# Kernel tuning notes

Hardware: AMD Instinct MI355X
Metric: run time of the kernel (lower is better)

## Reference

```python
import jax, jax.numpy as jnp
import numpy as np


def setup_inputs() -> dict:
    key = jax.random.key(0)
    ks = jax.random.split(key, 6)
    B, L, D, E = 4, 2048, 1024, 4
    H = 4 * D
    x = jax.random.normal(ks[0], (B, L, D), dtype=jnp.float32)
    # router: Linear(D, 2D) -> GELU -> Linear(2D, E); kaiming-ish init
    rW1 = jax.random.normal(ks[1], (D, 2 * D), dtype=jnp.float32) * (2.0 / D) ** 0.5
    rb1 = jnp.zeros((2 * D,), dtype=jnp.float32)
    rW2 = jax.random.normal(ks[2], (2 * D, E), dtype=jnp.float32) * (2.0 / (2 * D)) ** 0.5
    rb2 = jnp.zeros((E,), dtype=jnp.float32)
    # experts: Linear(D, 4D) -> GELU -> Linear(4D, D), stacked over E
    We1 = jax.random.normal(ks[3], (E, D, H), dtype=jnp.float32) * (2.0 / D) ** 0.5
    be1 = jnp.zeros((E, H), dtype=jnp.float32)
    We2 = jax.random.normal(ks[4], (E, H, D), dtype=jnp.float32) * (2.0 / H) ** 0.5
    be2 = jnp.zeros((E, D), dtype=jnp.float32)
    return {"x": x, "rW1": rW1, "rb1": rb1, "rW2": rW2, "rb2": rb2,
            "We1": We1, "be1": be1, "We2": We2, "be2": be2}


def reference(x, rW1, rb1, rW2, rb2, We1, be1, We2, be2):
    E = We1.shape[0]
    top_k = min(2, E)
    # router (dropouts are identity in eval mode)
    rh = jax.nn.gelu(x @ rW1 + rb1, approximate=False)          # [B,L,2D]
    router_logits = rh @ rW2 + rb2                               # [B,L,E]
    router_probs = jax.nn.softmax(router_logits, axis=-1)
    expert_weights, expert_indices = jax.lax.top_k(router_probs, top_k)  # [B,L,k]
    one_hot = jax.nn.one_hot(expert_indices, E, dtype=x.dtype)   # [B,L,k,E]
    token_mask = one_hot.sum(axis=2)                             # [B,L,E] 1 if expert selected
    combine_w = (one_hot * expert_weights[..., None]).sum(axis=2)  # [B,L,E] gate weight per expert
    out = jnp.zeros_like(x)
    for e in range(E):  # fixed small expert count; dense per-expert MLP over all tokens (as original)
        xi = x * token_mask[..., e:e + 1]
        h = jax.nn.gelu(xi @ We1[e] + be1[e], approximate=False)  # [B,L,4D]
        yo = h @ We2[e] + be2[e]                                  # [B,L,D]
        out = out + yo * combine_w[..., e:e + 1]
    return out
```

## Files before the change

### kernel.cpp

```cpp
#include <hip/hip_runtime.h>
#include <math.h>


typedef short bf16x8 __attribute__((ext_vector_type(8)));
typedef float f32x4 __attribute__((ext_vector_type(4)));
typedef unsigned short u16;

__device__ __forceinline__ u16 f2bf(float f) {
  unsigned u = __float_as_uint(f);
  u += 0x7FFFu + ((u >> 16) & 1u);
  return (u16)(u >> 16);
}
__device__ __forceinline__ float bf2f(u16 s) {
  return __uint_as_float(((unsigned)s) << 16);
}
__device__ __forceinline__ float gelu_f(float x) {
  return 0.5f * x * (1.0f + erff(x * 0.70710678118654752f));
}
__device__ __forceinline__ float gelu_fast(float x) {
  float y = 1.5957691216057308f * (x + 0.044715f * x * x * x);
  float e = __expf(y);
  float t = 1.0f - 2.0f * __builtin_amdgcn_rcpf(e + 1.0f);
  return 0.5f * x * (1.0f + t);
}
__device__ __forceinline__ void gload_lds16(const void* g, void* l) {
  __builtin_amdgcn_global_load_lds(
      (const __attribute__((address_space(1))) void*)g,
      (__attribute__((address_space(3))) void*)l, 16, 0, 0);
}

__global__ __launch_bounds__(256) void convert_split_kernel(
    const float* __restrict__ in, u16* __restrict__ hi, u16* __restrict__ lo,
    int n4) {
  int i = blockIdx.x * blockDim.x + threadIdx.x;
  int stride = gridDim.x * blockDim.x;
  for (; i < n4; i += stride) {
    float4 v = ((const float4*)in)[i];
    float f[4] = {v.x, v.y, v.z, v.w};
    ushort4 h4, l4;
    u16* hp = (u16*)&h4;
    u16* lp = (u16*)&l4;
#pragma unroll
    for (int u = 0; u < 4; ++u) {
      u16 h = f2bf(f[u]);
      hp[u] = h;
      lp[u] = f2bf(f[u] - bf2f(h));
    }
    ((ushort4*)hi)[i] = h4;
    ((ushort4*)lo)[i] = l4;
  }
}

__global__ __launch_bounds__(256) void transpose_split_kernel(
    const float* __restrict__ in, u16* __restrict__ hi, u16* __restrict__ lo,
    int R, int C) {
  __shared__ float tile[32][33];
  const int c0 = blockIdx.x * 32, r0 = blockIdx.y * 32;
#pragma unroll
  for (int i = 0; i < 4; ++i) {
    int rr = threadIdx.y + i * 8;
    tile[rr][threadIdx.x] = in[(size_t)(r0 + rr) * C + c0 + threadIdx.x];
  }
  __syncthreads();
#pragma unroll
  for (int i = 0; i < 4; ++i) {
    int cc = threadIdx.y + i * 8;
    float v = tile[threadIdx.x][cc];
    u16 h = f2bf(v);
    size_t oidx = (size_t)(c0 + cc) * R + r0 + threadIdx.x;
    hi[oidx] = h;
    lo[oidx] = f2bf(v - bf2f(h));
  }
}

__global__ __launch_bounds__(256) void transpose_pair_kernel(
    const float* __restrict__ We1, const float* __restrict__ We2,
    u16* __restrict__ T1, u16* __restrict__ T2, size_t tstride, int e0) {
  __shared__ float tile[32][33];
  const int e = e0 + blockIdx.y;
  int b = blockIdx.x;
  const float* in;
  u16* out;
  int R, C, tx, ty;
  if (b < 4096) {
    in = We1 + (size_t)e * 1024 * 4096;
    out = T1 + (size_t)blockIdx.y * tstride;
    R = 1024; C = 4096; tx = b & 127; ty = b >> 7;
  } else {
    b -= 4096;
    in = We2 + (size_t)e * 1024 * 4096;
    out = T2 + (size_t)blockIdx.y * tstride;
    R = 4096; C = 1024; tx = b & 31; ty = b >> 5;
  }
  const int c0 = tx * 32, r0 = ty * 32;
#pragma unroll
  for (int i = 0; i < 4; ++i) {
    int rr = threadIdx.y + i * 8;
    tile[rr][threadIdx.x] = in[(size_t)(r0 + rr) * C + c0 + threadIdx.x];
  }
  __syncthreads();
#pragma unroll
  for (int i = 0; i < 4; ++i) {
    int cc = threadIdx.y + i * 8;
    out[(size_t)(c0 + cc) * R + r0 + threadIdx.x] = f2bf(tile[threadIdx.x][cc]);
  }
}

__global__ __launch_bounds__(256) void gemm3_router_kernel(
    const u16* __restrict__ Ahi, const u16* __restrict__ Alo,
    const u16* __restrict__ Bhi, const u16* __restrict__ Blo, int K,
    const float* __restrict__ bias, const float* __restrict__ rW2,
    float* __restrict__ parts) {
  __shared__ alignas(16) u16 Sm[4 * 128 * 32];
  __shared__ float pls[2][128][4];
  const int tid = threadIdx.x;
  const int lane = tid & 63;
  const int w = tid >> 6;
  const int wr = w >> 1, wc = w & 1;

  const int flat = blockIdx.x + blockIdx.y * 16;
  const int swz = (flat & 7) * 128 + (flat >> 3);
  const int bxs = swz & 15;
  const int bys = swz >> 4;
  const int brow = bys * 128;
  const int bcol = bxs * 128;

  f32x4 acc[4][4] = {};
  char* S = (char*)Sm;
  const u16* srcs[4] = {Ahi + (size_t)brow * K, Alo + (size_t)brow * K,
                        Bhi + (size_t)bcol * K, Blo + (size_t)bcol * K};
  const int rA = lane & 15;
  const int kg2 = (lane >> 4) * 16;

  const int nk = K >> 5;
  for (int kt = 0; kt < nk; ++kt) {
    const int k0 = kt << 5;
    __syncthreads();
#pragma unroll
    for (int i = 0; i < 8; ++i) {
      int c = tid + 256 * i;
      int tile = c >> 9;
      int cc = c & 511;
      int row = cc >> 2;
      int kp = (cc & 3) << 3;
      gload_lds16(srcs[tile] + (size_t)row * K + (k0 + kp), S + c * 16);
    }
    __syncthreads();

    bf16x8 ah[4], al[4], bh[4], bl[4];
#pragma unroll
    for (int m = 0; m < 4; ++m) {
      int ro = (wr * 64 + m * 16 + rA) * 64 + kg2;
      ah[m] = *(const bf16x8*)(S + ro);
      al[m] = *(const bf16x8*)(S + 8192 + ro);
    }
#pragma unroll
    for (int n = 0; n < 4; ++n) {
      int ro = (wc * 64 + n * 16 + rA) * 64 + kg2;
      bh[n] = *(const bf16x8*)(S + 16384 + ro);
      bl[n] = *(const bf16x8*)(S + 24576 + ro);
    }
#pragma unroll
    for (int m = 0; m < 4; ++m)
#pragma unroll
      for (int n = 0; n < 4; ++n) {
        acc[m][n] = __builtin_amdgcn_mfma_f32_16x16x32_bf16(ah[m], bh[n], acc[m][n], 0, 0, 0);
        acc[m][n] = __builtin_amdgcn_mfma_f32_16x16x32_bf16(al[m], bh[n], acc[m][n], 0, 0, 0);
        acc[m][n] = __builtin_amdgcn_mfma_f32_16x16x32_bf16(ah[m], bl[n], acc[m][n], 0, 0, 0);
      }
  }

  const int cr = (lane >> 4) * 4;
  const int ccx = lane & 15;
  float4 w2v[4];
  float bv[4];
#pragma unroll
  for (int n = 0; n < 4; ++n) {
    const int gc = bcol + wc * 64 + n * 16 + ccx;
    w2v[n] = ((const float4*)rW2)[gc];
    bv[n] = bias[gc];
  }
#pragma unroll
  for (int m = 0; m < 4; ++m) {
    float pl[4][4];
#pragma unroll
    for (int r = 0; r < 4; ++r)
#pragma unroll
      for (int e = 0; e < 4; ++e) pl[r][e] = 0.f;
#pragma unroll
    for (int n = 0; n < 4; ++n)
#pragma unroll
      for (int r = 0; r < 4; ++r) {
        const float v = gelu_f(acc[m][n][r] + bv[n]);
        pl[r][0] += v * w2v[n].x;
        pl[r][1] += v * w2v[n].y;
        pl[r][2] += v * w2v[n].z;
        pl[r][3] += v * w2v[n].w;
      }
#pragma unroll
    for (int off = 8; off; off >>= 1)
#pragma unroll
      for (int r = 0; r < 4; ++r)
#pragma unroll
        for (int e = 0; e < 4; ++e) pl[r][e] += __shfl_xor(pl[r][e], off);
    if ((lane & 15) == 0) {
      const int row = wr * 64 + m * 16 + cr;
#pragma unroll
      for (int r = 0; r < 4; ++r)
#pragma unroll
        for (int e = 0; e < 4; ++e) pls[wc][row + r][e] = pl[r][e];
    }
  }
  __syncthreads();
  for (int i = tid; i < 512; i += 256) {
    const int row = i >> 2, e = i & 3;
    parts[((size_t)bxs * 8192 + brow + row) * 4 + e] =
        pls[0][row][e] + pls[1][row][e];
  }
}

__global__ __launch_bounds__(256) void topk_kernel(
    const float* __restrict__ parts, const float* __restrict__ rb2,
    float* __restrict__ combine, int* __restrict__ cnt, int* __restrict__ list,
    int T) {
  const int t = blockIdx.x * 256 + threadIdx.x;
  const int w = threadIdx.x >> 6, lane = threadIdx.x & 63;
  __shared__ int wpre[4][4];
  __shared__ int gbase[4];

  float lg[4] = {rb2[0], rb2[1], rb2[2], rb2[3]};
#pragma unroll
  for (int s = 0; s < 16; ++s) {
    float4 pv = ((const float4*)parts)[(size_t)s * 8192 + t];
    lg[0] += pv.x;
    lg[1] += pv.y;
    lg[2] += pv.z;
    lg[3] += pv.w;
  }
  float mx = fmaxf(fmaxf(lg[0], lg[1]), fmaxf(lg[2], lg[3]));
  float p[4], sum = 0.f;
#pragma unroll
  for (int e = 0; e < 4; ++e) {
    p[e] = expf(lg[e] - mx);
    sum += p[e];
  }
  float inv = 1.0f / sum;
  int i1 = 0;
#pragma unroll
  for (int e = 1; e < 4; ++e)
    if (lg[e] > lg[i1]) i1 = e;
  int i2 = -1;
#pragma unroll
  for (int e = 0; e < 4; ++e)
    if (e != i1 && (i2 < 0 || lg[e] > lg[i2])) i2 = e;
  float4 cw = {0.f, 0.f, 0.f, 0.f};
  ((float*)&cw)[i1] = p[i1] * inv;
  ((float*)&cw)[i2] = p[i2] * inv;
  ((float4*)combine)[t] = cw;

  unsigned long long m[4];
#pragma unroll
  for (int e = 0; e < 4; ++e) m[e] = __ballot(i1 == e || i2 == e);
  if (lane == 0) {
#pragma unroll
    for (int e = 0; e < 4; ++e) wpre[w][e] = (int)__popcll(m[e]);
  }
  __syncthreads();
  if (threadIdx.x < 4) {
    const int e = threadIdx.x;
    int tot = 0;
#pragma unroll
    for (int ww = 0; ww < 4; ++ww) {
      int c = wpre[ww][e];
      wpre[ww][e] = tot;
      tot += c;
    }
    gbase[e] = atomicAdd(&cnt[e], tot);
  }
  __syncthreads();
  const unsigned long long lt = (1ull << lane) - 1ull;
  int p1 = gbase[i1] + wpre[w][i1] + (int)__popcll(m[i1] & lt);
  list[i1 * 8192 + p1] = t;
  int p2 = gbase[i2] + wpre[w][i2] + (int)__popcll(m[i2] & lt);
  list[i2 * 8192 + p2] = t;
}

__global__ void prefix_kernel(const int* __restrict__ cnt, int* __restrict__ pre) {
  if (threadIdx.x == 0) {
    int s = 0;
#pragma unroll
    for (int e = 0; e < 4; ++e) {
      pre[e] = s;
      s += cnt[e];
    }
  }
}

__global__ __launch_bounds__(512) void gemm_gather_kernel(
    const u16* __restrict__ A, const u16* __restrict__ WT, size_t wts,
    const int* __restrict__ list, const int* __restrict__ cnt_arr,
    const int* __restrict__ hbase_arr, int e0, const float* __restrict__ be1,
    u16* __restrict__ h) {
  const int K = 1024;
  const int e = e0 + blockIdx.z;
  const int cnt = cnt_arr[e];
  const int rb = blockIdx.y;
  if (rb * 128 >= cnt) return;
  const int hbase = hbase_arr[e];
  const int* lst = list + e * 8192;
  const u16* Bt = WT + (size_t)blockIdx.z * wts;
  const float* bias = be1 + e * 4096;

  __shared__ alignas(16) u16 As[128 * 64];
  __shared__ alignas(16) u16 Bs[256 * 64];
  const int tid = threadIdx.x;
  const int lane = tid & 63;
  const int w = tid >> 6;
  const int wr = w >> 2, wc = w & 3;
  const int bcol = blockIdx.x * 256;

  const int srow = tid >> 3;
  const int jx8 = (((tid & 7) ^ (srow & 7)) << 3);
  const u16* aS[2];
  const u16* bS[4];
#pragma unroll
  for (int i = 0; i < 2; ++i) {
    int g = rb * 128 + srow + 64 * i;
    int tok = lst[(g < cnt) ? g : rb * 128];
    aS[i] = A + (size_t)tok * K + jx8;
  }
#pragma unroll
  for (int i = 0; i < 4; ++i)
    bS[i] = Bt + (size_t)(bcol + srow + 64 * i) * K + jx8;
  char* AsB = (char*)As;
  char* BsB = (char*)Bs;
  const int dstb = tid * 16;

  f32x4 acc[4][4] = {};
  const int rA = lane & 15;
  const int ksl = lane >> 4;
  const int rx7 = rA & 7;

  const int nk = K >> 6;
  for (int kt = 0; kt < nk; ++kt) {
    const int kb = kt << 6;
    __syncthreads();
#pragma unroll
    for (int i = 0; i < 2; ++i)
      gload_lds16(aS[i] + kb, AsB + i * 8192 + dstb);
#pragma unroll
    for (int i = 0; i < 4; ++i)
      gload_lds16(bS[i] + kb, BsB + i * 8192 + dstb);
    __syncthreads();
#pragma unroll
    for (int s = 0; s < 2; ++s) {
      bf16x8 a[4], b[4];
      const int sl = (((s * 4 + ksl) ^ rx7) << 4);
#pragma unroll
      for (int m = 0; m < 4; ++m)
        a[m] = *(const bf16x8*)(AsB + (wr * 64 + m * 16 + rA) * 128 + sl);
#pragma unroll
      for (int n = 0; n < 4; ++n)
        b[n] = *(const bf16x8*)(BsB + (wc * 64 + n * 16 + rA) * 128 + sl);
#pragma unroll
      for (int m = 0; m < 4; ++m)
#pragma unroll
        for (int n = 0; n < 4; ++n)
          acc[m][n] =
              __builtin_amdgcn_mfma_f32_16x16x32_bf16(a[m], b[n], acc[m][n], 0, 0, 0);
    }
  }

  const int cr = (lane >> 4) * 4;
  const int ccx = lane & 15;
#pragma unroll
  for (int m = 0; m < 4; ++m)
#pragma unroll
    for (int n = 0; n < 4; ++n) {
      const int gc = bcol + wc * 64 + n * 16 + ccx;
      const float bv = bias[gc];
#pragma unroll
      for (int r = 0; r < 4; ++r) {
        const int gl = rb * 128 + wr * 64 + m * 16 + cr + r;
        if (gl < cnt)
          h[(size_t)(hbase + gl) * 4096 + gc] = f2bf(gelu_fast(acc[m][n][r] + bv));
      }
    }
}

__global__ __launch_bounds__(512) void gemm_scatter_kernel(
    const u16* __restrict__ h, const int* __restrict__ hbase_arr,
    const u16* __restrict__ WT, size_t wts, const int* __restrict__ list,
    const int* __restrict__ cnt_arr, int e0, const float* __restrict__ be2,
    const float* __restrict__ combine, float* __restrict__ out) {
  const int K = 4096;
  const int zslot = blockIdx.z >> 1;
  const int kz = blockIdx.z & 1;
  const int e = e0 + zslot;
  const int cnt = cnt_arr[e];
  const int rb = blockIdx.y;
  if (rb * 128 >= cnt) return;
  const int hbase = hbase_arr[e];
  const int* lst = list + e * 8192;
  const u16* Bt = WT + (size_t)zslot * wts;
  const float* bias = be2 + e * 1024;
  const int koff = kz * 2048;

  __shared__ alignas(16) u16 As[128 * 64];
  __shared__ alignas(16) u16 Bs[256 * 64];
  const int tid = threadIdx.x;
  const int lane = tid & 63;
  const int w = tid >> 6;
  const int wr = w >> 2, wc = w & 3;
  const int bcol = blockIdx.x * 256;

  const int srow = tid >> 3;
  const int jx8 = (((tid & 7) ^ (srow & 7)) << 3);
  const u16* aS[2];
  const u16* bS[4];
#pragma unroll
  for (int i = 0; i < 2; ++i)
    aS[i] = h + (size_t)(hbase + rb * 128 + srow + 64 * i) * K + koff + jx8;
#pragma unroll
  for (int i = 0; i < 4; ++i)
    bS[i] = Bt + (size_t)(bcol + srow + 64 * i) * K + koff + jx8;
  char* AsB = (char*)As;
  char* BsB = (char*)Bs;
  const int dstb = tid * 16;

  f32x4 acc[4][4] = {};
  const int rA = lane & 15;
  const int ksl = lane >> 4;
  const int rx7 = rA & 7;

  const int nk = 2048 >> 6;
  for (int kt = 0; kt < nk; ++kt) {
    const int kb = kt << 6;
    __syncthreads();
#pragma unroll
    for (int i = 0; i < 2; ++i)
      gload_lds16(aS[i] + kb, AsB + i * 8192 + dstb);
#pragma unroll
    for (int i = 0; i < 4; ++i)
      gload_lds16(bS[i] + kb, BsB + i * 8192 + dstb);
    __syncthreads();
#pragma unroll
    for (int s = 0; s < 2; ++s) {
      bf16x8 a[4], b[4];
      const int sl = (((s * 4 + ksl) ^ rx7) << 4);
#pragma unroll
      for (int m = 0; m < 4; ++m)
        a[m] = *(const bf16x8*)(AsB + (wr * 64 + m * 16 + rA) * 128 + sl);
#pragma unroll
      for (int n = 0; n < 4; ++n)
        b[n] = *(const bf16x8*)(BsB + (wc * 64 + n * 16 + rA) * 128 + sl);
#pragma unroll
      for (int m = 0; m < 4; ++m)
#pragma unroll
        for (int n = 0; n < 4; ++n)
          acc[m][n] =
              __builtin_amdgcn_mfma_f32_16x16x32_bf16(a[m], b[n], acc[m][n], 0, 0, 0);
    }
  }

  const int cr = (lane >> 4) * 4;
  const int ccx = lane & 15;
  const bool addb = (kz == 0);
#pragma unroll
  for (int m = 0; m < 4; ++m)
#pragma unroll
    for (int r = 0; r < 4; ++r) {
      const int gl = rb * 128 + wr * 64 + m * 16 + cr + r;
      if (gl >= cnt) continue;
      const int tok = lst[gl];
      const float gcoef = combine[(size_t)tok * 4 + e];
      float* orow = out + (size_t)tok * 1024;
#pragma unroll
      for (int n = 0; n < 4; ++n) {
        const int gc = bcol + wc * 64 + n * 16 + ccx;
        float v = acc[m][n][r];
        if (addb) v += bias[gc];
        atomicAdd(&orow[gc], gcoef * v);
      }
    }
}

extern "C" void kernel_launch(void* const* d_in, const int* in_sizes, int n_in,
                              void* d_out, int out_size, void* d_ws,
                              size_t ws_size, hipStream_t stream) {
  const float* x = (const float*)d_in[0];
  const float* rW1 = (const float*)d_in[1];
  const float* rb1 = (const float*)d_in[2];
  const float* rW2 = (const float*)d_in[3];
  const float* rb2 = (const float*)d_in[4];
  const float* We1 = (const float*)d_in[5];
  const float* be1 = (const float*)d_in[6];
  const float* We2 = (const float*)d_in[7];
  const float* be2 = (const float*)d_in[8];
  float* out = (float*)d_out;

  const int T = 8192, D = 1024, D2 = 2048, H = 4096, E = 4;
  const size_t WTS = (size_t)H * D;

  char* ws = (char*)d_ws;
  size_t off = 0;
  auto alloc = [&](size_t bytes) {
    char* p = ws + off;
    off = (off + bytes + 255) & ~(size_t)255;
    return p;
  };
  u16* x_hi = (u16*)alloc((size_t)T * D * 2);
  float* combine = (float*)alloc((size_t)T * 4 * 4);
  int* cnt = (int*)alloc(256);
  int* prefix = cnt + 4;
  int* list = (int*)alloc((size_t)4 * 8192 * 4);
  const size_t common_off = off;

  bool merged;
  u16 *We1T, *We2T, *h, *x_lo, *rW1T_hi, *rW1T_lo;
  float* parts;
  {
    size_t o = common_off;
    auto a2 = [&](size_t bytes) {
      char* p = ws + o;
      o = (o + bytes + 255) & ~(size_t)255;
      return p;
    };
    u16* w1 = (u16*)a2((size_t)4 * WTS * 2);
    u16* w2 = (u16*)a2((size_t)4 * WTS * 2);
    char* hreg = a2((size_t)16384 * H * 2 + (2u << 20));
    merged = (o <= ws_size);
    if (merged) {
      We1T = w1;
      We2T = w2;
      h = (u16*)hreg;
      x_lo = (u16*)hreg;
      rW1T_hi = (u16*)(hreg + (16u << 20));
      rW1T_lo = (u16*)(hreg + (20u << 20));
      parts = (float*)(hreg + (24u << 20));
    }
  }
  if (!merged) {
    off = common_off;
    We1T = (u16*)alloc(WTS * 2);
    We2T = (u16*)alloc(WTS * 2);
    x_lo = (u16*)alloc((size_t)T * D * 2);
    rW1T_hi = (u16*)alloc((size_t)D2 * D * 2);
    rW1T_lo = (u16*)alloc((size_t)D2 * D * 2);
    parts = (float*)alloc((size_t)16 * T * 4 * 4);
    h = (u16*)alloc((size_t)T * H * 2);
  }

  hipMemsetAsync(cnt, 0, 32, stream);
  hipMemsetAsync(out, 0, (size_t)T * D * 4, stream);

  dim3 tb(32, 8);

  convert_split_kernel<<<2048, 256, 0, stream>>>(x, x_hi, x_lo, T * D / 4);
  transpose_split_kernel<<<dim3(D2 / 32, D / 32), tb, 0, stream>>>(
      rW1, rW1T_hi, rW1T_lo, D, D2);
  gemm3_router_kernel<<<dim3(16, 64), 256, 0, stream>>>(
      x_hi, x_lo, rW1T_hi, rW1T_lo, D, rb1, rW2, parts);
  topk_kernel<<<T / 256, 256, 0, stream>>>(parts, rb2, combine, cnt, list, T);

  if (merged) {
    prefix_kernel<<<1, 64, 0, stream>>>(cnt, prefix);
    transpose_pair_kernel<<<dim3(8192, 4), tb, 0, stream>>>(
        We1, We2, We1T, We2T, WTS, 0);
    gemm_gather_kernel<<<dim3(16, 64, 4), 512, 0, stream>>>(
        x_hi, We1T, WTS, list, cnt, prefix, 0, be1, h);
    gemm_scatter_kernel<<<dim3(4, 64, 8), 512, 0, stream>>>(
        h, prefix, We2T, WTS, list, cnt, 0, be2, combine, out);
  } else {
    for (int e = 0; e < E; ++e) {
      transpose_pair_kernel<<<dim3(8192, 1), tb, 0, stream>>>(
          We1, We2, We1T, We2T, 0, e);
      gemm_gather_kernel<<<dim3(16, 64, 1), 512, 0, stream>>>(
          x_hi, We1T, 0, list, cnt, prefix , e, be1, h);
      gemm_scatter_kernel<<<dim3(4, 64, 2), 512, 0, stream>>>(
          h, prefix , We2T, 0, list, cnt, e, be2, combine, out);
    }
  }
}
```

Before: 603.0 us.

## Replace atomic scatter with per-slot expert output buffer plus combine kernel

The second expert GEMM now writes each expert's outputs densely into a slot-ordered buffer instead of atomically accumulating gated results into the output with split-K. A new combine kernel uses a per-token slot map recorded in top-k to gather both expert rows and apply the gate weights. This removes atomics, split-K, and the output memset. The cost is extra workspace and an additional full read/write pass, and a larger workspace may make the merged path unavailable.

```diff
diff --git a/kernel.cpp b/kernel.cpp
--- a/kernel.cpp
+++ b/kernel.cpp
@@ -222,7 +222,7 @@
 __global__ __launch_bounds__(256) void topk_kernel(
     const float* __restrict__ parts, const float* __restrict__ rb2,
     float* __restrict__ combine, int* __restrict__ cnt, int* __restrict__ list,
-    int T) {
+    int2* __restrict__ tokslot, int T) {
   const int t = blockIdx.x * 256 + threadIdx.x;
   const int w = threadIdx.x >> 6, lane = threadIdx.x & 63;
   __shared__ int wpre[4][4];
@@ -283,6 +283,7 @@
   list[i1 * 8192 + p1] = t;
   int p2 = gbase[i2] + wpre[w][i2] + (int)__popcll(m[i2] & lt);
   list[i2 * 8192 + p2] = t;
+  tokslot[t] = make_int2(i1 * 8192 + p1, i2 * 8192 + p2);
 }
 
 __global__ void prefix_kernel(const int* __restrict__ cnt, int* __restrict__ pre) {
@@ -386,6 +387,121 @@
           h[(size_t)(hbase + gl) * 4096 + gc] = f2bf(gelu_fast(acc[m][n][r] + bv));
       }
     }
+}
+
+__global__ __launch_bounds__(512) void gemm_scatter_y_kernel(
+    const u16* __restrict__ h, const int* __restrict__ hbase_arr,
+    const u16* __restrict__ WT, size_t wts, const int* __restrict__ cnt_arr,
+    int e0, const float* __restrict__ be2, float* __restrict__ yout) {
+  const int K = 4096;
+  const int e = e0 + blockIdx.z;
+  const int cnt = cnt_arr[e];
+  const int rb = blockIdx.y;
+  if (rb * 128 >= cnt) return;
+  const int hbase = hbase_arr[e];
+  const u16* Bt = WT + (size_t)blockIdx.z * wts;
+  const float* bias = be2 + e * 1024;
+
+  __shared__ alignas(16) u16 As[128 * 64];
+  __shared__ alignas(16) u16 Bs[256 * 64];
+  const int tid = threadIdx.x;
+  const int lane = tid & 63;
+  const int w = tid >> 6;
+  const int wr = w >> 2, wc = w & 3;
+  const int bcol = blockIdx.x * 256;
+
+  const int srow = tid >> 3;
+  const int jx8 = (((tid & 7) ^ (srow & 7)) << 3);
+  const u16* aS[2];
+  const u16* bS[4];
+#pragma unroll
+  for (int i = 0; i < 2; ++i)
+    aS[i] = h + (size_t)(hbase + rb * 128 + srow + 64 * i) * K + jx8;
+#pragma unroll
+  for (int i = 0; i < 4; ++i)
+    bS[i] = Bt + (size_t)(bcol + srow + 64 * i) * K + jx8;
+  char* AsB = (char*)As;
+  char* BsB = (char*)Bs;
+  const int dstb = tid * 16;
+
+  f32x4 acc[4][4] = {};
+  const int rA = lane & 15;
+  const int ksl = lane >> 4;
+  const int rx7 = rA & 7;
+
+  const int nk = K >> 6;
+  for (int kt = 0; kt < nk; ++kt) {
+    const int kb = kt << 6;
+    __syncthreads();
+#pragma unroll
+    for (int i = 0; i < 2; ++i)
+      gload_lds16(aS[i] + kb, AsB + i * 8192 + dstb);
+#pragma unroll
+    for (int i = 0; i < 4; ++i)
+      gload_lds16(bS[i] + kb, BsB + i * 8192 + dstb);
+    __syncthreads();
+#pragma unroll
+    for (int s = 0; s < 2; ++s) {
+      bf16x8 a[4], b[4];
+      const int sl = (((s * 4 + ksl) ^ rx7) << 4);
+#pragma unroll
+      for (int m = 0; m < 4; ++m)
+        a[m] = *(const bf16x8*)(AsB + (wr * 64 + m * 16 + rA) * 128 + sl);
+#pragma unroll
+      for (int n = 0; n < 4; ++n)
+        b[n] = *(const bf16x8*)(BsB + (wc * 64 + n * 16 + rA) * 128 + sl);
+#pragma unroll
+      for (int m = 0; m < 4; ++m)
+#pragma unroll
+        for (int n = 0; n < 4; ++n)
+          acc[m][n] =
+              __builtin_amdgcn_mfma_f32_16x16x32_bf16(a[m], b[n], acc[m][n], 0, 0, 0);
+    }
+  }
+
+  const int cr = (lane >> 4) * 4;
+  const int ccx = lane & 15;
+#pragma unroll
+  for (int m = 0; m < 4; ++m)
+#pragma unroll
+    for (int r = 0; r < 4; ++r) {
+      const int gl = rb * 128 + wr * 64 + m * 16 + cr + r;
+      if (gl >= cnt) continue;
+      float* yrow = yout + (size_t)(hbase + gl) * 1024;
+#pragma unroll
+      for (int n = 0; n < 4; ++n) {
+        const int gc = bcol + wc * 64 + n * 16 + ccx;
+        yrow[gc] = acc[m][n][r] + bias[gc];
+      }
+    }
+}
+
+__global__ __launch_bounds__(256) void combine_kernel(
+    const float* __restrict__ yout, const int2* __restrict__ tokslot,
+    const int* __restrict__ prefix, const float* __restrict__ gates,
+    float* __restrict__ out) {
+  const int w = threadIdx.x >> 6, lane = threadIdx.x & 63;
+  const int t = blockIdx.x * 4 + w;
+  const int2 s = tokslot[t];
+  const int e1 = s.x >> 13, p1 = s.x & 8191;
+  const int e2 = s.y >> 13, p2 = s.y & 8191;
+  const int r1 = prefix[e1] + p1;
+  const int r2 = prefix[e2] + p2;
+  const float g1 = gates[(size_t)t * 4 + e1];
+  const float g2 = gates[(size_t)t * 4 + e2];
+  const float4* y1 = (const float4*)(yout + (size_t)r1 * 1024);
+  const float4* y2 = (const float4*)(yout + (size_t)r2 * 1024);
+  float4* o = (float4*)(out + (size_t)t * 1024);
+#pragma unroll
+  for (int j = 0; j < 4; ++j) {
+    const int c = lane + j * 64;
+    float4 a = y1[c], b = y2[c], r;
+    r.x = g1 * a.x + g2 * b.x;
+    r.y = g1 * a.y + g2 * b.y;
+    r.z = g1 * a.z + g2 * b.z;
+    r.w = g1 * a.w + g2 * b.w;
+    o[c] = r;
+  }
 }
 
 __global__ __launch_bounds__(512) void gemm_scatter_kernel(
@@ -514,11 +630,12 @@
   int* cnt = (int*)alloc(256);
   int* prefix = cnt + 4;
   int* list = (int*)alloc((size_t)4 * 8192 * 4);
+  int2* tokslot = (int2*)alloc((size_t)T * 8);
   const size_t common_off = off;
 
   bool merged;
   u16 *We1T, *We2T, *h, *x_lo, *rW1T_hi, *rW1T_lo;
-  float* parts;
+  float *parts, *yout;
   {
     size_t o = common_off;
     auto a2 = [&](size_t bytes) {
@@ -529,11 +646,13 @@
     u16* w1 = (u16*)a2((size_t)4 * WTS * 2);
     u16* w2 = (u16*)a2((size_t)4 * WTS * 2);
     char* hreg = a2((size_t)16384 * H * 2 + (2u << 20));
+    float* yo = (float*)a2((size_t)16384 * 1024 * 4);
     merged = (o <= ws_size);
     if (merged) {
       We1T = w1;
       We2T = w2;
       h = (u16*)hreg;
+      yout = yo;
       x_lo = (u16*)hreg;
       rW1T_hi = (u16*)(hreg + (16u << 20));
       rW1T_lo = (u16*)(hreg + (20u << 20));
@@ -549,10 +668,11 @@
     rW1T_lo = (u16*)alloc((size_t)D2 * D * 2);
     parts = (float*)alloc((size_t)16 * T * 4 * 4);
     h = (u16*)alloc((size_t)T * H * 2);
+    yout = nullptr;
   }
 
   hipMemsetAsync(cnt, 0, 32, stream);
-  hipMemsetAsync(out, 0, (size_t)T * D * 4, stream);
+  if (!merged) hipMemsetAsync(out, 0, (size_t)T * D * 4, stream);
 
   dim3 tb(32, 8);
 
@@ -561,7 +681,8 @@
       rW1, rW1T_hi, rW1T_lo, D, D2);
   gemm3_router_kernel<<<dim3(16, 64), 256, 0, stream>>>(
       x_hi, x_lo, rW1T_hi, rW1T_lo, D, rb1, rW2, parts);
-  topk_kernel<<<T / 256, 256, 0, stream>>>(parts, rb2, combine, cnt, list, T);
+  topk_kernel<<<T / 256, 256, 0, stream>>>(parts, rb2, combine, cnt, list,
+                                           tokslot, T);
 
   if (merged) {
     prefix_kernel<<<1, 64, 0, stream>>>(cnt, prefix);
@@ -569,8 +690,10 @@
         We1, We2, We1T, We2T, WTS, 0);
     gemm_gather_kernel<<<dim3(16, 64, 4), 512, 0, stream>>>(
         x_hi, We1T, WTS, list, cnt, prefix, 0, be1, h);
-    gemm_scatter_kernel<<<dim3(4, 64, 8), 512, 0, stream>>>(
-        h, prefix, We2T, WTS, list, cnt, 0, be2, combine, out);
+    gemm_scatter_y_kernel<<<dim3(4, 64, 4), 512, 0, stream>>>(
+        h, prefix, We2T, WTS, cnt, 0, be2, yout);
+    combine_kernel<<<T / 4, 256, 0, stream>>>(yout, tokslot, prefix, combine,
+                                              out);
   } else {
     for (int e = 0; e < E; ++e) {
       transpose_pair_kernel<<<dim3(8192, 1), tb, 0, stream>>>(
```

Result: slower. 770.1 us (+27.7%).
